# Kernel tuning notes

Hardware: AMD Instinct MI355X
Metric: run time of the kernel (lower is better)

## Reference

```python
import jax, jax.numpy as jnp
import numpy as np

RES = 64
EPS = 1e-6


def _maps_to_kp(front_vec, front_dis, back_vec, back_dis, ske_mask):
    # front_vec/back_vec: [B,20,res,res,2]; front_dis/back_dis/ske_mask: [B,20,res,res,1]
    B = front_vec.shape[0]
    xs = jnp.arange(RES, dtype=front_vec.dtype)
    # torch builds locs with locs[:, x, y, 0]=x, locs[:, x, y, 1]=y
    locs = jnp.stack(jnp.meshgrid(xs, xs, indexing='ij'), axis=-1)  # [res,res,2]

    def vote_sum(vec, dis, mask):
        # masked weighted spatial sum, normalized by mask mass (the torch
        # `if sum(mask)!=0` guard is a no-op: zero mask -> zero votes)
        votes = mask * (vec * dis * RES + locs)        # [B,20,res,res,2]
        num = jnp.sum(votes, axis=(2, 3))              # [B,20,2]
        den = jnp.sum(mask, axis=(2, 3)) + EPS         # [B,20,1]
        return num / den

    front_sum = vote_sum(front_vec, front_dis, ske_mask)  # [B,20,2]
    back_sum = vote_sum(back_vec, back_dis, ske_mask)     # [B,20,2]

    # keypoint 0 (wrist): average of back predictions at channels 0,4,8,12,16
    kp0 = jnp.mean(back_sum[:, ::4], axis=1)              # [B,2]

    # channel c = 4*i + j maps to keypoint t = 4*i + 4 - j (t in 1..20)
    c = jnp.arange(20)
    j = c % 4
    t = 4 * (c // 4) + 4 - j
    back_next = jnp.roll(back_sum, -1, axis=1)            # back_sum[:, c+1]; c%4==3 slots unused
    vals = jnp.where((j == 3)[None, :, None], front_sum,
                     (front_sum + back_next) * 0.5)       # [B,20,2]

    kp = jnp.zeros((B, 21, 2), front_vec.dtype)
    kp = kp.at[:, 0].set(kp0)
    kp = kp.at[:, t].set(vals)
    return kp * 4.0


def setup_inputs() -> dict:
    key = jax.random.key(0)
    k1, k2, k3, k4, k5 = jax.random.split(key, 5)
    B = 256
    return {
        'front_vec': jax.random.normal(k1, (B, 20, RES, RES, 2), dtype=jnp.float32),
        'front_dis': jax.random.uniform(k2, (B, 20, RES, RES, 1), dtype=jnp.float32),
        'back_vec': jax.random.normal(k3, (B, 20, RES, RES, 2), dtype=jnp.float32),
        'back_dis': jax.random.uniform(k4, (B, 20, RES, RES, 1), dtype=jnp.float32),
        'ske_mask': jax.random.uniform(k5, (B, 20, RES, RES, 1), dtype=jnp.float32),
    }


def reference(front_vec, front_dis, back_vec, back_dis, ske_mask):
    return _maps_to_kp(front_vec, front_dis, back_vec, back_dis, ske_mask)
```

## Files before the change

kernel.cpp:

```cpp
#include <hip/hip_runtime.h>

#define NCH 20
#define RESOLUTION 64
#define PTS (RESOLUTION * RESOLUTION)

__global__ __launch_bounds__(256, 1) void vote_reduce(
    const float4* __restrict__ fv, const float4* __restrict__ fd,
    const float4* __restrict__ bv, const float4* __restrict__ bd,
    const float4* __restrict__ mk, float* __restrict__ sums)
{
    const int slab = blockIdx.x;
    const int tid  = threadIdx.x;

    const float4* fvp = fv + (size_t)slab * (PTS * 2 / 4);
    const float4* bvp = bv + (size_t)slab * (PTS * 2 / 4);
    const float4* fdp = fd + (size_t)slab * (PTS / 4);
    const float4* bdp = bd + (size_t)slab * (PTS / 4);
    const float4* mkp = mk + (size_t)slab * (PTS / 4);

    float4 m4[4], fd4[4], bd4[4], fva[4], fvb[4], bva[4], bvb[4];
    #pragma unroll
    for (int g = 0; g < 4; ++g) {
        const int i = g * 256 + tid;
        fva[g] = fvp[2 * i];
        fvb[g] = fvp[2 * i + 1];
        bva[g] = bvp[2 * i];
        bvb[g] = bvp[2 * i + 1];
        fd4[g] = fdp[i];
        bd4[g] = bdp[i];
        m4[g]  = mkp[i];
    }

    __builtin_amdgcn_sched_barrier(0);

    float fnx = 0.f, fny = 0.f, bnx = 0.f, bny = 0.f, den = 0.f;
    #pragma unroll
    for (int g = 0; g < 4; ++g) {
        const int i = g * 256 + tid;
        const float mm [4] = { m4[g].x,  m4[g].y,  m4[g].z,  m4[g].w  };
        const float fdd[4] = { fd4[g].x, fd4[g].y, fd4[g].z, fd4[g].w };
        const float bdd[4] = { bd4[g].x, bd4[g].y, bd4[g].z, bd4[g].w };
        const float fvx[4] = { fva[g].x, fva[g].z, fvb[g].x, fvb[g].z };
        const float fvy[4] = { fva[g].y, fva[g].w, fvb[g].y, fvb[g].w };
        const float bvx[4] = { bva[g].x, bva[g].z, bvb[g].x, bvb[g].z };
        const float bvy[4] = { bva[g].y, bva[g].w, bvb[g].y, bvb[g].w };

        const int p0 = i * 4;
        #pragma unroll
        for (int q = 0; q < 4; ++q) {
            const int p  = p0 + q;
            const float x = (float)(p >> 6);
            const float y = (float)(p & 63);
            const float m = mm[q];
            fnx += m * (fvx[q] * fdd[q] * 64.f + x);
            fny += m * (fvy[q] * fdd[q] * 64.f + y);
            bnx += m * (bvx[q] * bdd[q] * 64.f + x);
            bny += m * (bvy[q] * bdd[q] * 64.f + y);
            den += m;
        }
    }

    #pragma unroll
    for (int off = 32; off > 0; off >>= 1) {
        fnx += __shfl_down(fnx, off);
        fny += __shfl_down(fny, off);
        bnx += __shfl_down(bnx, off);
        bny += __shfl_down(bny, off);
        den += __shfl_down(den, off);
    }

    __shared__ float red[4][5];
    const int wave = tid >> 6;
    const int lane = tid & 63;
    if (lane == 0) {
        red[wave][0] = fnx; red[wave][1] = fny;
        red[wave][2] = bnx; red[wave][3] = bny;
        red[wave][4] = den;
    }
    __syncthreads();
    if (tid == 0) {
        float s0 = 0.f, s1 = 0.f, s2 = 0.f, s3 = 0.f, s4 = 0.f;
        #pragma unroll
        for (int w = 0; w < 4; ++w) {
            s0 += red[w][0]; s1 += red[w][1];
            s2 += red[w][2]; s3 += red[w][3];
            s4 += red[w][4];
        }
        float* o = sums + (size_t)slab * 5;
        o[0] = s0; o[1] = s1; o[2] = s2; o[3] = s3; o[4] = s4;
    }
}

__global__ __launch_bounds__(64) void combine(
    const float* __restrict__ sums, float* __restrict__ out, int B)
{
    const int b = blockIdx.x * blockDim.x + threadIdx.x;
    if (b >= B) return;

    float fsx[NCH], fsy[NCH], bsx[NCH], bsy[NCH];
    #pragma unroll
    for (int c = 0; c < NCH; ++c) {
        const float* s = sums + (size_t)(b * NCH + c) * 5;
        const float inv = 1.f / (s[4] + 1e-6f);
        fsx[c] = s[0] * inv; fsy[c] = s[1] * inv;
        bsx[c] = s[2] * inv; bsy[c] = s[3] * inv;
    }

    const float k0x = 0.2f * (bsx[0] + bsx[4] + bsx[8] + bsx[12] + bsx[16]);
    const float k0y = 0.2f * (bsy[0] + bsy[4] + bsy[8] + bsy[12] + bsy[16]);

    float* o = out + (size_t)b * 42;
    o[0] = k0x * 4.f;
    o[1] = k0y * 4.f;

    #pragma unroll
    for (int c = 0; c < NCH; ++c) {
        const int j = c & 3;
        const int t = (c & ~3) + 4 - j;
        float vx, vy;
        if (j == 3) {
            vx = fsx[c]; vy = fsy[c];
        } else {
            vx = 0.5f * (fsx[c] + bsx[c + 1]);
            vy = 0.5f * (fsy[c] + bsy[c + 1]);
        }
        o[t * 2]     = vx * 4.f;
        o[t * 2 + 1] = vy * 4.f;
    }
}

extern "C" void kernel_launch(void* const* d_in, const int* in_sizes, int n_in,
                              void* d_out, int out_size, void* d_ws, size_t ws_size,
                              hipStream_t stream) {
    const float4* fv = (const float4*)d_in[0];
    const float4* fd = (const float4*)d_in[1];
    const float4* bv = (const float4*)d_in[2];
    const float4* bd = (const float4*)d_in[3];
    const float4* mk = (const float4*)d_in[4];

    const int B = in_sizes[0] / (NCH * PTS * 2);
    float* sums = (float*)d_ws;
    float* out  = (float*)d_out;

    vote_reduce<<<B * NCH, 256, 0, stream>>>(fv, fd, bv, bd, mk, sums);
    combine<<<(B + 63) / 64, 64, 0, stream>>>(sums, out, B);
}
```

Before: 103.4 us.

## Split each slab across two blocks and hand-pipeline loads with inline asm

Each channel slab is now split across two blocks, each covering half the points, which doubles the grid size. Partial sums are written per half and merged in the combine kernel. Loads are issued as inline-asm global_load_dwordx4 instructions, with explicit s_waitcnt so the first half's arithmetic starts while the second half's loads are still in flight. The change adds more blocks and a larger workspace, and relies on manual vmcnt bookkeeping being correct.

New measurement: 104.8 us. About the same (+1.3%).

```diff
diff --git a/kernel.cpp b/kernel.cpp
--- a/kernel.cpp
+++ b/kernel.cpp
@@ -1,64 +1,88 @@
 #include <hip/hip_runtime.h>
 
 #define NCH 20
-#define RESOLUTION 64
-#define PTS (RESOLUTION * RESOLUTION)
+#define PTS 4096
+
+typedef float f32x4 __attribute__((ext_vector_type(4)));
+
+#define GL(dst, base, voff, imm) \
+    asm volatile("global_load_dwordx4 %0, %1, %2 offset:" #imm \
+                 : "=v"(dst) : "v"(voff), "s"(base))
 
 __global__ __launch_bounds__(256, 1) void vote_reduce(
-    const float4* __restrict__ fv, const float4* __restrict__ fd,
-    const float4* __restrict__ bv, const float4* __restrict__ bd,
-    const float4* __restrict__ mk, float* __restrict__ sums)
+    const float* __restrict__ fv, const float* __restrict__ fd,
+    const float* __restrict__ bv, const float* __restrict__ bd,
+    const float* __restrict__ mk, float* __restrict__ sums)
 {
-    const int slab = blockIdx.x;
+    const int bid  = blockIdx.x;
+    const int slab = bid >> 1;
+    const int half = bid & 1;
     const int tid  = threadIdx.x;
 
-    const float4* fvp = fv + (size_t)slab * (PTS * 2 / 4);
-    const float4* bvp = bv + (size_t)slab * (PTS * 2 / 4);
-    const float4* fdp = fd + (size_t)slab * (PTS / 4);
-    const float4* bdp = bd + (size_t)slab * (PTS / 4);
-    const float4* mkp = mk + (size_t)slab * (PTS / 4);
+    const float* fvp = fv + (size_t)slab * (PTS * 2);
+    const float* bvp = bv + (size_t)slab * (PTS * 2);
+    const float* fdp = fd + (size_t)slab * PTS;
+    const float* bdp = bd + (size_t)slab * PTS;
+    const float* mkp = mk + (size_t)slab * PTS;
 
-    float4 m4[4], fd4[4], bd4[4], fva[4], fvb[4], bva[4], bvb[4];
-    #pragma unroll
-    for (int g = 0; g < 4; ++g) {
-        const int i = g * 256 + tid;
-        fva[g] = fvp[2 * i];
-        fvb[g] = fvp[2 * i + 1];
-        bva[g] = bvp[2 * i];
-        bvb[g] = bvp[2 * i + 1];
-        fd4[g] = fdp[i];
-        bd4[g] = bdp[i];
-        m4[g]  = mkp[i];
+    const int i0 = half * 512 + tid;
+    const int i1 = i0 + 256;
+    const unsigned off16_0 = (unsigned)i0 * 16u;
+    const unsigned off32_0 = (unsigned)i0 * 32u;
+    const unsigned off16_1 = (unsigned)i1 * 16u;
+    const unsigned off32_1 = (unsigned)i1 * 32u;
+
+    f32x4 FVA0, FVB0, BVA0, BVB0, FD0, BD0, M0;
+    f32x4 FVA1, FVB1, BVA1, BVB1, FD1, BD1, M1;
+
+    GL(FVA0, fvp, off32_0, 0);
+    GL(FVB0, fvp, off32_0, 16);
+    GL(BVA0, bvp, off32_0, 0);
+    GL(BVB0, bvp, off32_0, 16);
+    GL(FD0,  fdp, off16_0, 0);
+    GL(BD0,  bdp, off16_0, 0);
+    GL(M0,   mkp, off16_0, 0);
+    GL(FVA1, fvp, off32_1, 0);
+    GL(FVB1, fvp, off32_1, 16);
+    GL(BVA1, bvp, off32_1, 0);
+    GL(BVB1, bvp, off32_1, 16);
+    GL(FD1,  fdp, off16_1, 0);
+    GL(BD1,  bdp, off16_1, 0);
+    GL(M1,   mkp, off16_1, 0);
+
+    float fnx = 0.f, fny = 0.f, bnx = 0.f, bny = 0.f, den = 0.f;
+
+#define CONSUME(FVA, FVB, BVA, BVB, FD4, BD4, M4, I)                         \
+    {                                                                        \
+        const float mm [4] = { M4.x,  M4.y,  M4.z,  M4.w  };                 \
+        const float fdd[4] = { FD4.x, FD4.y, FD4.z, FD4.w };                 \
+        const float bdd[4] = { BD4.x, BD4.y, BD4.z, BD4.w };                 \
+        const float fvx[4] = { FVA.x, FVA.z, FVB.x, FVB.z };                 \
+        const float fvy[4] = { FVA.y, FVA.w, FVB.y, FVB.w };                 \
+        const float bvx[4] = { BVA.x, BVA.z, BVB.x, BVB.z };                 \
+        const float bvy[4] = { BVA.y, BVA.w, BVB.y, BVB.w };                 \
+        const int p0 = (I) * 4;                                              \
+        _Pragma("unroll")                                                    \
+        for (int q = 0; q < 4; ++q) {                                        \
+            const int p  = p0 + q;                                           \
+            const float x = (float)(p >> 6);            \
+            const float y = (float)(p & 63);            \
+            const float m = mm[q];                                           \
+            fnx += m * (fvx[q] * fdd[q] * 64.f + x);                         \
+            fny += m * (fvy[q] * fdd[q] * 64.f + y);                         \
+            bnx += m * (bvx[q] * bdd[q] * 64.f + x);                         \
+            bny += m * (bvy[q] * bdd[q] * 64.f + y);                         \
+            den += m;                                                        \
+        }                                                                    \
     }
 
+    asm volatile("s_waitcnt vmcnt(7)" ::: "memory");
     __builtin_amdgcn_sched_barrier(0);
+    CONSUME(FVA0, FVB0, BVA0, BVB0, FD0, BD0, M0, i0);
 
-    float fnx = 0.f, fny = 0.f, bnx = 0.f, bny = 0.f, den = 0.f;
-    #pragma unroll
-    for (int g = 0; g < 4; ++g) {
-        const int i = g * 256 + tid;
-        const float mm [4] = { m4[g].x,  m4[g].y,  m4[g].z,  m4[g].w  };
-        const float fdd[4] = { fd4[g].x, fd4[g].y, fd4[g].z, fd4[g].w };
-        const float bdd[4] = { bd4[g].x, bd4[g].y, bd4[g].z, bd4[g].w };
-        const float fvx[4] = { fva[g].x, fva[g].z, fvb[g].x, fvb[g].z };
-        const float fvy[4] = { fva[g].y, fva[g].w, fvb[g].y, fvb[g].w };
-        const float bvx[4] = { bva[g].x, bva[g].z, bvb[g].x, bvb[g].z };
-        const float bvy[4] = { bva[g].y, bva[g].w, bvb[g].y, bvb[g].w };
-
-        const int p0 = i * 4;
-        #pragma unroll
-        for (int q = 0; q < 4; ++q) {
-            const int p  = p0 + q;
-            const float x = (float)(p >> 6);
-            const float y = (float)(p & 63);
-            const float m = mm[q];
-            fnx += m * (fvx[q] * fdd[q] * 64.f + x);
-            fny += m * (fvy[q] * fdd[q] * 64.f + y);
-            bnx += m * (bvx[q] * bdd[q] * 64.f + x);
-            bny += m * (bvy[q] * bdd[q] * 64.f + y);
-            den += m;
-        }
-    }
+    asm volatile("s_waitcnt vmcnt(0)" ::: "memory");
+    __builtin_amdgcn_sched_barrier(0);
+    CONSUME(FVA1, FVB1, BVA1, BVB1, FD1, BD1, M1, i1);
 
     #pragma unroll
     for (int off = 32; off > 0; off >>= 1) {
@@ -86,7 +110,7 @@
             s2 += red[w][2]; s3 += red[w][3];
             s4 += red[w][4];
         }
-        float* o = sums + (size_t)slab * 5;
+        float* o = sums + ((size_t)slab * 2 + half) * 5;
         o[0] = s0; o[1] = s1; o[2] = s2; o[3] = s3; o[4] = s4;
     }
 }
@@ -100,10 +124,13 @@
     float fsx[NCH], fsy[NCH], bsx[NCH], bsy[NCH];
     #pragma unroll
     for (int c = 0; c < NCH; ++c) {
-        const float* s = sums + (size_t)(b * NCH + c) * 5;
-        const float inv = 1.f / (s[4] + 1e-6f);
-        fsx[c] = s[0] * inv; fsy[c] = s[1] * inv;
-        bsx[c] = s[2] * inv; bsy[c] = s[3] * inv;
+        const float* s = sums + (size_t)(b * NCH + c) * 10;
+        const float den = s[4] + s[9];
+        const float inv = 1.f / (den + 1e-6f);
+        fsx[c] = (s[0] + s[5]) * inv;
+        fsy[c] = (s[1] + s[6]) * inv;
+        bsx[c] = (s[2] + s[7]) * inv;
+        bsy[c] = (s[3] + s[8]) * inv;
     }
 
     const float k0x = 0.2f * (bsx[0] + bsx[4] + bsx[8] + bsx[12] + bsx[16]);
@@ -132,16 +159,16 @@
 extern "C" void kernel_launch(void* const* d_in, const int* in_sizes, int n_in,
                               void* d_out, int out_size, void* d_ws, size_t ws_size,
                               hipStream_t stream) {
-    const float4* fv = (const float4*)d_in[0];
-    const float4* fd = (const float4*)d_in[1];
-    const float4* bv = (const float4*)d_in[2];
-    const float4* bd = (const float4*)d_in[3];
-    const float4* mk = (const float4*)d_in[4];
+    const float* fv = (const float*)d_in[0];
+    const float* fd = (const float*)d_in[1];
+    const float* bv = (const float*)d_in[2];
+    const float* bd = (const float*)d_in[3];
+    const float* mk = (const float*)d_in[4];
 
     const int B = in_sizes[0] / (NCH * PTS * 2);
     float* sums = (float*)d_ws;
     float* out  = (float*)d_out;
 
-    vote_reduce<<<B * NCH, 256, 0, stream>>>(fv, fd, bv, bd, mk, sums);
+    vote_reduce<<<B * NCH * 2, 256, 0, stream>>>(fv, fd, bv, bd, mk, sums);
     combine<<<(B + 63) / 64, 64, 0, stream>>>(sums, out, B);
 }
```
